# Kernel optimization log

Measured on AMD Instinct MI355X. Metric: run time of the kernel, lower is better.

The kernel has to match this reference:

```python
import jax, jax.numpy as jnp
import numpy as np

HID = 256  # hidden_dim in the torch module


def _graph_conv(h, edges, W0, b0, W1, b1):
    # pytorch3d.ops.GraphConv (undirected): out = w0(h) + sum_{neighbors} w1(h_nbr),
    # where each edge (i, j) contributes in both directions.
    out = h @ W0 + b0          # [V, H]
    nbr = h @ W1 + b1          # [V, H]
    i, j = edges[:, 0], edges[:, 1]
    out = out.at[i].add(nbr[j])
    out = out.at[j].add(nbr[i])
    return out


def setup_inputs() -> dict:
    key = jax.random.key(0)
    ks = jax.random.split(key, 16)
    V, E, F, H = 20496, 61440, 3840, HID  # 8 meshes x (2562 verts, 7680 edges); F = 256+512+1024+2048

    def w(k, shape):
        return jax.random.normal(k, shape, dtype=jnp.float32) * 0.02

    return {
        "vert_img_feats": jax.random.normal(ks[0], (V, F), dtype=jnp.float32),
        "verts": jax.random.normal(ks[1], (V, 3), dtype=jnp.float32),
        "edges": jax.random.randint(ks[2], (E, 2), 0, V),
        # bottleneck Linear(3840 -> 256)
        "Wb": w(ks[3], (F, H)), "bb": jnp.zeros((H,), jnp.float32),
        # GraphConv 0: input_dim = 3 + 256
        "W0_0": w(ks[4], (3 + H, H)), "b0_0": jnp.zeros((H,), jnp.float32),
        "W1_0": w(ks[5], (3 + H, H)), "b1_0": jnp.zeros((H,), jnp.float32),
        # GraphConv 1..9 stacked
        "gW0": w(ks[6], (9, H, H)), "gb0": jnp.zeros((9, H), jnp.float32),
        "gW1": w(ks[7], (9, H, H)), "gb1": jnp.zeros((9, H), jnp.float32),
        # vert_offset Linear(256 -> 3)
        "Wo": w(ks[8], (H, 3)), "bo": jnp.zeros((3,), jnp.float32),
        # asym_conf MLP: 256 -> 256 -> 64 -> 32 -> 1
        "A1": w(ks[9], (H, H)), "a1": jnp.zeros((H,), jnp.float32),
        "A2": w(ks[10], (H, 64)), "a2": jnp.zeros((64,), jnp.float32),
        "A3": w(ks[11], (64, 32)), "a3": jnp.zeros((32,), jnp.float32),
        "A4": w(ks[12], (32, 1)), "a4": jnp.zeros((1,), jnp.float32),
    }


def reference(vert_img_feats, verts, edges, Wb, bb, W0_0, b0_0, W1_0, b1_0,
              gW0, gb0, gW1, gb1, Wo, bo, A1, a1, A2, a2, A3, a3, A4, a4):
    # bottleneck + ReLU on per-vertex image features (vert_align output)
    h_img = jax.nn.relu(vert_img_feats @ Wb + bb)            # [V, 256]
    h = jnp.concatenate([h_img, verts], axis=1)              # [V, 259]
    h = jax.nn.relu(_graph_conv(h, edges, W0_0, b0_0, W1_0, b1_0))
    for k in range(9):  # fixed layer count, structurally distinct params
        h = jax.nn.relu(_graph_conv(h, edges, gW0[k], gb0[k], gW1[k], gb1[k]))
    delta_v = h @ Wo + bo                                    # [V, 3]
    z = jax.nn.relu(h @ A1 + a1)
    z = jax.nn.relu(z @ A2 + a2)
    z = jax.nn.relu(z @ A3 + a3)
    asym_conf = jax.nn.sigmoid(z @ A4 + a4)                  # [V, 1]
    return delta_v, asym_conf
```

## Files before the change

kernel.cpp:

```cpp
#include <hip/hip_runtime.h>

typedef _Float16 half8  __attribute__((ext_vector_type(8)));
typedef _Float16 half4v __attribute__((ext_vector_type(4)));
typedef float    floatx4 __attribute__((ext_vector_type(4)));

#define DEVINL __device__ __forceinline__

DEVINL void async_cp16(const void* g, void* l){
  __builtin_amdgcn_global_load_lds(
      (const __attribute__((address_space(1))) void*)g,
      (__attribute__((address_space(3))) void*)l,
      16, 0, 0);
}

DEVINL float wred64(float x){
  #pragma unroll
  for (int m = 32; m; m >>= 1) x += __shfl_xor(x, m, 64);
  return x;
}

__global__ __launch_bounds__(256) void k_gemm_bb(
    const float* __restrict__ A, const _Float16* __restrict__ BT,
    float* __restrict__ P, int M, int Mpad, int K, int lda, int kChunk)
{
  constexpr int BM = 128, BK = 32;
  __shared__ alignas(16) float    As[BM * BK];
  __shared__ alignas(16) _Float16 Bs[BM * BK];
  const int tid = threadIdx.x, wid = tid >> 6, lane = tid & 63;
  const int bm = blockIdx.x, bn = blockIdx.y, bz = blockIdx.z;
  const int kbeg = bz * kChunk, kend = kbeg + kChunk;

  const float* aSrc[4]; float* aDst[4];
  const int uSwA = (lane & 7) ^ ((lane >> 3) & 7);
  #pragma unroll
  for (int c = 0; c < 4; c++){
    int rloc = wid * 32 + c * 8 + (lane >> 3);
    int r = min(bm * BM + rloc, M - 1);
    aSrc[c] = A + (size_t)r * lda + uSwA * 4;
    aDst[c] = &As[(wid * 32 + c * 8) * BK];
  }
  const _Float16* bSrc[2]; _Float16* bDst[2];
  const int uSwB = (lane & 3) ^ ((lane >> 2) & 3);
  #pragma unroll
  for (int s = 0; s < 2; s++){
    int rb = bn * BM + (wid * 2 + s) * 16 + (lane >> 2);
    bSrc[s] = BT + (size_t)rb * K + uSwB * 8;
    bDst[s] = &Bs[(wid * 2 + s) * 16 * BK];
  }

  floatx4 acc[4][4];
  #pragma unroll
  for (int mt = 0; mt < 4; mt++)
    #pragma unroll
    for (int nt = 0; nt < 4; nt++) acc[mt][nt] = {0.f, 0.f, 0.f, 0.f};

  const int arow0 = (wid >> 1) * 64 + (lane & 15);
  const int g2 = (lane >> 4) * 2;
  const int a7 = lane & 7;
  const int brow0 = (wid & 1) * 64 + (lane & 15);
  const int ub = (lane >> 4) ^ (lane & 3);

  for (int k0 = kbeg; k0 < kend; k0 += BK){
    __syncthreads();
    #pragma unroll
    for (int c = 0; c < 4; c++) async_cp16(aSrc[c] + k0, aDst[c]);
    #pragma unroll
    for (int s = 0; s < 2; s++) async_cp16(bSrc[s] + k0, bDst[s]);
    __syncthreads();
    half8 af[4], bf[4];
    #pragma unroll
    for (int mt = 0; mt < 4; mt++){
      int arow = arow0 + mt * 16;
      floatx4 lo = *(const floatx4*)&As[arow * BK + ((g2    ) ^ a7) * 4];
      floatx4 hi = *(const floatx4*)&As[arow * BK + ((g2 + 1) ^ a7) * 4];
      #pragma unroll
      for (int j = 0; j < 4; j++){ af[mt][j] = (_Float16)lo[j]; af[mt][4+j] = (_Float16)hi[j]; }
    }
    #pragma unroll
    for (int nt = 0; nt < 4; nt++)
      bf[nt] = *(const half8*)&Bs[(brow0 + nt * 16) * BK + ub * 8];
    #pragma unroll
    for (int mt = 0; mt < 4; mt++)
      #pragma unroll
      for (int nt = 0; nt < 4; nt++)
        acc[mt][nt] = __builtin_amdgcn_mfma_f32_16x16x32_f16(af[mt], bf[nt], acc[mt][nt], 0, 0, 0);
  }

  const int colLocal = (wid & 1) * 64 + (lane & 15);
  const int rowLocal = (wid >> 1) * 64 + (lane >> 4) * 4;
  float* Pz = P + (size_t)bz * Mpad * 256;
  #pragma unroll
  for (int nt = 0; nt < 4; nt++){
    int col = bn * BM + colLocal + nt * 16;
    #pragma unroll
    for (int mt = 0; mt < 4; mt++){
      int r0 = bm * BM + rowLocal + mt * 16;
      #pragma unroll
      for (int i = 0; i < 4; i++)
        Pz[(size_t)(r0 + i) * 256 + col] = acc[mt][nt][i];
    }
  }
}

__global__ __launch_bounds__(256) void k_reduce(
    const float* __restrict__ P, const float* __restrict__ bias,
    _Float16* __restrict__ hA, int V, int Mpad)
{
  int idx = blockIdx.x * 256 + threadIdx.x;
  int base = idx * 4;
  int r = base >> 8, c = base & 255;
  const size_t stride = (size_t)Mpad * 256;
  const float* p = P + (size_t)r * 256 + c;
  floatx4 s0 = *(const floatx4*)(p);
  floatx4 s1 = *(const floatx4*)(p + stride);
  floatx4 s2 = *(const floatx4*)(p + 2 * stride);
  floatx4 s3 = *(const floatx4*)(p + 3 * stride);
  floatx4 b = *(const floatx4*)(bias + c);
  half4v o;
  if (r < V){
    #pragma unroll
    for (int e = 0; e < 4; e++)
      o[e] = (_Float16)fmaxf(s0[e] + s1[e] + s2[e] + s3[e] + b[e], 0.f);
  } else {
    #pragma unroll
    for (int e = 0; e < 4; e++) o[e] = (_Float16)0.f;
  }
  *(half4v*)(hA + (size_t)r * 256 + c) = o;
}

template<bool RELU, bool SPLIT, bool VERTC>
__global__ __launch_bounds__(256) void k_conv(
    const _Float16* __restrict__ A,
    const _Float16* __restrict__ BTfrag,
    const float* __restrict__ bias0, const float* __restrict__ bias1,
    const float* __restrict__ vertW, const float* __restrict__ verts,
    _Float16* __restrict__ C0, _Float16* __restrict__ C1, int Vreal)
{
  __shared__ alignas(16) _Float16 Bs[32768];
  const int tid = threadIdx.x, wid = tid >> 6, lane = tid & 63;
  const int bm = blockIdx.x, bn = blockIdx.y;

  const _Float16* src = BTfrag + (size_t)bn * 32768;
  #pragma unroll
  for (int jj = 0; jj < 16; jj++){
    int e = (jj * 256 + tid) * 8;
    *(half8*)&Bs[e] = *(const half8*)&src[e];
  }
  __syncthreads();

  const _Float16* Arow[4];
  #pragma unroll
  for (int mt = 0; mt < 4; mt++)
    Arow[mt] = A + (size_t)(bm * 128 + (wid >> 1) * 64 + mt * 16 + (lane & 15)) * 256
                 + (lane >> 4) * 8;
  const int nbase = (wid & 1) * 4;

  floatx4 acc[4][4];
  #pragma unroll
  for (int mt = 0; mt < 4; mt++)
    #pragma unroll
    for (int nt = 0; nt < 4; nt++) acc[mt][nt] = {0.f, 0.f, 0.f, 0.f};

  #pragma unroll
  for (int j = 0; j < 8; j++){
    half8 af[4], bf[4];
    #pragma unroll
    for (int mt = 0; mt < 4; mt++) af[mt] = *(const half8*)(Arow[mt] + j * 32);
    #pragma unroll
    for (int nt = 0; nt < 4; nt++)
      bf[nt] = *(const half8*)&Bs[(((nbase + nt) * 8 + j) * 64 + lane) * 8];
    #pragma unroll
    for (int mt = 0; mt < 4; mt++)
      #pragma unroll
      for (int nt = 0; nt < 4; nt++)
        acc[mt][nt] = __builtin_amdgcn_mfma_f32_16x16x32_f16(af[mt], bf[nt], acc[mt][nt], 0, 0, 0);
  }

  const int colLocal = (wid & 1) * 64 + (lane & 15);
  const int rowLocal = (wid >> 1) * 64 + (lane >> 4) * 4;
  #pragma unroll
  for (int nt = 0; nt < 4; nt++){
    int g = bn * 128 + colLocal + nt * 16;
    _Float16* Cp = C0;
    const float* bp = bias0;
    int col = g;
    if (SPLIT && g >= 256){ Cp = C1; bp = bias1; col = g - 256; }
    float b = bp[col];
    float w0 = 0.f, w1 = 0.f, w2 = 0.f;
    if (VERTC){ w0 = vertW[g*3+0]; w1 = vertW[g*3+1]; w2 = vertW[g*3+2]; }
    #pragma unroll
    for (int mt = 0; mt < 4; mt++){
      int r0 = bm * 128 + rowLocal + mt * 16;
      #pragma unroll
      for (int i = 0; i < 4; i++){
        int r = r0 + i;
        float v = acc[mt][nt][i] + b;
        if (VERTC){
          int vr = min(r, Vreal - 1);
          v += verts[vr*3+0] * w0 + verts[vr*3+1] * w1 + verts[vr*3+2] * w2;
        }
        if (RELU) v = fmaxf(v, 0.f);
        Cp[(size_t)r * 256 + col] = (_Float16)v;
      }
    }
  }
}

__global__ __launch_bounds__(256) void k_fill(const int* __restrict__ e, int E,
                                              int* __restrict__ cnt, int* __restrict__ adj){
  int t = blockIdx.x * 256 + threadIdx.x;
  if (t >= E) return;
  int i = e[t*2], j = e[t*2+1];
  int s = atomicAdd(&cnt[i], 1); if (s < 64) adj[(size_t)i*64 + s] = j;
  int q = atomicAdd(&cnt[j], 1); if (q < 64) adj[(size_t)j*64 + q] = i;
}

__global__ __launch_bounds__(256) void k_trans_bb(
    const float* __restrict__ Wb, _Float16* __restrict__ WbT)
{
  __shared__ float T[64][65];
  const int k0 = blockIdx.x * 64, n0 = blockIdx.y * 64;
  const int tr = threadIdx.x >> 6, tc = threadIdx.x & 63;
  #pragma unroll
  for (int i = 0; i < 16; i++){
    int rr = i * 4 + tr;
    T[rr][tc] = Wb[(size_t)(k0 + rr) * 256 + n0 + tc];
  }
  __syncthreads();
  #pragma unroll
  for (int i = 0; i < 16; i++){
    int rr = i * 4 + tr;
    WbT[(size_t)(n0 + rr) * 3840 + k0 + tc] = (_Float16)T[tc][rr];
  }
}

__global__ __launch_bounds__(256) void k_pack_frag(
    const float* __restrict__ W0_0, const float* __restrict__ W1_0,
    const float* __restrict__ gW0,  const float* __restrict__ gW1,
    const float* __restrict__ A1,
    _Float16* __restrict__ convB, _Float16* __restrict__ A1T,
    float* __restrict__ vertW)
{
  if (blockIdx.x == 672){
    for (int i = threadIdx.x; i < 1536; i += 256){
      int n = i / 3, c = i % 3;
      vertW[i] = (n < 256) ? W0_0[(size_t)(256 + c) * 256 + n]
                           : W1_0[(size_t)(256 + c) * 256 + (n - 256)];
    }
    return;
  }
  const int gw = blockIdx.x * 4 + (threadIdx.x >> 6);
  const int lane = threadIdx.x & 63;
  if (gw < 2560){
    int L = gw >> 8;
    int r = gw & 255;
    int n = (r >> 3) * 16 + (lane & 15);
    int k = (r & 7) * 32 + (lane >> 4) * 8;
    const float* W0 = L ? gW0 + (size_t)(L - 1) * 65536 : W0_0;
    const float* W1 = L ? gW1 + (size_t)(L - 1) * 65536 : W1_0;
    const float* Wsel = (n < 256) ? W0 : W1;
    int nn = n & 255;
    half8 v;
    #pragma unroll
    for (int e = 0; e < 8; e++) v[e] = (_Float16)Wsel[(size_t)(k + e) * 256 + nn];
    *(half8*)&convB[(size_t)L * 131072 + (size_t)r * 512 + lane * 8] = v;
  } else {
    int r = gw - 2560;
    int n = (r >> 3) * 16 + (lane & 15);
    int k = (r & 7) * 32 + (lane >> 4) * 8;
    half8 v;
    #pragma unroll
    for (int e = 0; e < 8; e++) v[e] = (_Float16)A1[(size_t)(k + e) * 256 + n];
    *(half8*)&A1T[(size_t)r * 512 + lane * 8] = v;
  }
}

__global__ __launch_bounds__(256) void k_gather(
    const _Float16* __restrict__ outB, const _Float16* __restrict__ nbrB,
    const int* __restrict__ cnt, const int* __restrict__ adj,
    _Float16* __restrict__ h, int V)
{
  int gw = (int)((blockIdx.x * 256 + threadIdx.x) >> 6);
  int lane = threadIdx.x & 63;
  if (gw >= V) return;
  half4v o = ((const half4v*)(outB + (size_t)gw * 256))[lane];
  float a0 = (float)o[0], a1 = (float)o[1], a2 = (float)o[2], a3 = (float)o[3];
  int n = min(cnt[gw], 64);
  const int* ap = adj + (size_t)gw * 64;
  int d = 0;
  for (; d + 1 < n; d += 2){
    int u0 = ap[d], u1 = ap[d+1];
    half4v x = ((const half4v*)(nbrB + (size_t)u0 * 256))[lane];
    half4v y = ((const half4v*)(nbrB + (size_t)u1 * 256))[lane];
    a0 += (float)x[0] + (float)y[0]; a1 += (float)x[1] + (float)y[1];
    a2 += (float)x[2] + (float)y[2]; a3 += (float)x[3] + (float)y[3];
  }
  if (d < n){
    int u = ap[d];
    half4v x = ((const half4v*)(nbrB + (size_t)u * 256))[lane];
    a0 += (float)x[0]; a1 += (float)x[1]; a2 += (float)x[2]; a3 += (float)x[3];
  }
  half4v rr;
  rr[0] = (_Float16)fmaxf(a0, 0.f); rr[1] = (_Float16)fmaxf(a1, 0.f);
  rr[2] = (_Float16)fmaxf(a2, 0.f); rr[3] = (_Float16)fmaxf(a3, 0.f);
  ((half4v*)(h + (size_t)gw * 256))[lane] = rr;
}

__global__ __launch_bounds__(1024) void k_head(
    const _Float16* __restrict__ hA, const _Float16* __restrict__ z1,
    const float* __restrict__ Wo, const float* __restrict__ bo,
    const float* __restrict__ A2, const float* __restrict__ a2,
    const float* __restrict__ A3, const float* __restrict__ a3,
    const float* __restrict__ A4, const float* __restrict__ a4,
    float* __restrict__ dOut, int V)
{
  __shared__ float A2s[256 * 64];
  __shared__ float A3s[64 * 32];
  __shared__ float Wos[768];
  __shared__ float zrow[16][256];
  __shared__ float z2s[16][64];
  const int tid = threadIdx.x;
  for (int i = tid; i < 256*64; i += 1024) A2s[i] = A2[i];
  for (int i = tid; i < 64*32;  i += 1024) A3s[i] = A3[i];
  if (tid < 768) Wos[tid] = Wo[tid];
  __syncthreads();
  const int wid = tid >> 6, lane = tid & 63;
  const int v = blockIdx.x * 16 + wid;
  if (v >= V) return;

  half4v hv = ((const half4v*)(hA + (size_t)v * 256))[lane];
  float hf[4] = { (float)hv[0], (float)hv[1], (float)hv[2], (float)hv[3] };
  float p0 = 0.f, p1 = 0.f, p2 = 0.f;
  int c0 = lane * 4;
  #pragma unroll
  for (int j = 0; j < 4; j++){
    p0 += hf[j] * Wos[(c0+j)*3 + 0];
    p1 += hf[j] * Wos[(c0+j)*3 + 1];
    p2 += hf[j] * Wos[(c0+j)*3 + 2];
  }
  p0 = wred64(p0); p1 = wred64(p1); p2 = wred64(p2);
  if (lane == 0){
    dOut[(size_t)v*3 + 0] = p0 + bo[0];
    dOut[(size_t)v*3 + 1] = p1 + bo[1];
    dOut[(size_t)v*3 + 2] = p2 + bo[2];
  }

  half4v zv = ((const half4v*)(z1 + (size_t)v * 256))[lane];
  floatx4 zf; zf[0] = (float)zv[0]; zf[1] = (float)zv[1]; zf[2] = (float)zv[2]; zf[3] = (float)zv[3];
  ((floatx4*)zrow[wid])[lane] = zf;
  __threadfence_block();
  float acc2 = a2[lane];
  #pragma unroll 4
  for (int c = 0; c < 256; c++) acc2 += zrow[wid][c] * A2s[c*64 + lane];
  acc2 = fmaxf(acc2, 0.f);
  z2s[wid][lane] = acc2;
  __threadfence_block();
  int o = lane & 31;
  float acc3 = a3[o];
  #pragma unroll 4
  for (int c = 0; c < 64; c++) acc3 += z2s[wid][c] * A3s[c*32 + o];
  acc3 = fmaxf(acc3, 0.f);
  float p = (lane < 32) ? acc3 * A4[lane] : 0.f;
  p = wred64(p);
  if (lane == 0){
    float s = 1.f / (1.f + expf(-(p + a4[0])));
    dOut[(size_t)V*3 + v] = s;
  }
}

extern "C" void kernel_launch(void* const* d_in, const int* in_sizes, int n_in,
                              void* d_out, int out_size, void* d_ws, size_t ws_size,
                              hipStream_t stream)
{
  const int V = 20496, E = 61440, F = 3840, Vpad = 20608;
  const float* X     = (const float*)d_in[0];
  const float* verts = (const float*)d_in[1];
  const int*   edges = (const int*)d_in[2];
  const float* Wb    = (const float*)d_in[3];
  const float* bbias = (const float*)d_in[4];
  const float* W0_0  = (const float*)d_in[5];
  const float* b0_0  = (const float*)d_in[6];
  const float* W1_0  = (const float*)d_in[7];
  const float* b1_0  = (const float*)d_in[8];
  const float* gW0   = (const float*)d_in[9];
  const float* gb0   = (const float*)d_in[10];
  const float* gW1   = (const float*)d_in[11];
  const float* gb1   = (const float*)d_in[12];
  const float* Wo    = (const float*)d_in[13];
  const float* bo    = (const float*)d_in[14];
  const float* A1    = (const float*)d_in[15];
  const float* a1    = (const float*)d_in[16];
  const float* A2    = (const float*)d_in[17];
  const float* a2    = (const float*)d_in[18];
  const float* A3    = (const float*)d_in[19];
  const float* a3    = (const float*)d_in[20];
  const float* A4    = (const float*)d_in[21];
  const float* a4    = (const float*)d_in[22];

  char* w = (char*)d_ws;
  const size_t SA = (size_t)Vpad * 256 * 2;
  _Float16* hA    = (_Float16*)(w);
  _Float16* outB  = (_Float16*)(w + SA);
  _Float16* nbrB  = (_Float16*)(w + 2*SA);
  _Float16* z1    = (_Float16*)(w + 3*SA);
  size_t off = 4 * SA;
  float*    P     = (float*)(w + off);    off += (size_t)4 * Vpad * 256 * 4;
  _Float16* WbT   = (_Float16*)(w + off); off += (size_t)256*3840*2;
  _Float16* convB = (_Float16*)(w + off); off += (size_t)10*131072*2;
  _Float16* A1T   = (_Float16*)(w + off); off += (size_t)131072*2;
  float*    vertW = (float*)(w + off);    off += (size_t)1536*4;
  int*      cnt   = (int*)(w + off);      off += (size_t)V*4;
  int*      adj   = (int*)(w + off);

  hipMemsetAsync(cnt, 0, (size_t)V*4, stream);

  k_fill<<<dim3((E + 255)/256), dim3(256), 0, stream>>>(edges, E, cnt, adj);
  k_trans_bb<<<dim3(60, 4), dim3(256), 0, stream>>>(Wb, WbT);
  k_pack_frag<<<dim3(673), dim3(256), 0, stream>>>(
      W0_0, W1_0, gW0, gW1, A1, convB, A1T, vertW);

  k_gemm_bb<<<dim3(161, 2, 4), dim3(256), 0, stream>>>(X, WbT, P, V, Vpad, F, F, 960);
  k_reduce<<<dim3(Vpad * 64 / 256), dim3(256), 0, stream>>>(P, bbias, hA, V, Vpad);

  for (int l = 0; l < 10; l++){
    const float* bp0 = l ? gb0 + (size_t)(l-1)*256 : b0_0;
    const float* bp1 = l ? gb1 + (size_t)(l-1)*256 : b1_0;
    const _Float16* Bt = convB + (size_t)l * 131072;
    if (l == 0)
      k_conv<false, true, true><<<dim3(161, 4), dim3(256), 0, stream>>>(
          hA, Bt, bp0, bp1, vertW, verts, outB, nbrB, V);
    else
      k_conv<false, true, false><<<dim3(161, 4), dim3(256), 0, stream>>>(
          hA, Bt, bp0, bp1, nullptr, nullptr, outB, nbrB, V);
    k_gather<<<dim3(5124), dim3(256), 0, stream>>>(outB, nbrB, cnt, adj, hA, V);
  }

  k_conv<true, false, false><<<dim3(161, 2), dim3(256), 0, stream>>>(
      hA, A1T, a1, nullptr, nullptr, nullptr, z1, nullptr, V);

  k_head<<<dim3(V/16), dim3(1024), 0, stream>>>(
      hA, z1, Wo, bo, A2, a2, A3, a3, A4, a4, (float*)d_out, V);
}
```

Measured before the change: 991.6 us.

## Widen bottleneck GEMM tile to full N, store fp16 partials, LDS-transpose weight packing

The bottleneck GEMM now computes all 256 output columns per block, so the large fp32 feature matrix is streamed and converted once instead of twice. Split-K partial sums are written in fp16, halving partial-buffer traffic in both the GEMM and the reduce kernel. Weight fragment packing is rewritten to stage weights through a shared-memory transpose with coalesced loads. The wider tile doubles accumulator registers per thread, which risks spills or lower occupancy, and fp16 partials reduce accumulation precision.

```diff
diff --git a/kernel.cpp b/kernel.cpp
--- a/kernel.cpp
+++ b/kernel.cpp
@@ -19,15 +19,15 @@
   return x;
 }
 
-__global__ __launch_bounds__(256) void k_gemm_bb(
+__global__ __launch_bounds__(256, 2) void k_gemm_bb(
     const float* __restrict__ A, const _Float16* __restrict__ BT,
-    float* __restrict__ P, int M, int Mpad, int K, int lda, int kChunk)
+    _Float16* __restrict__ P, int M, int Mpad, int K, int lda, int kChunk)
 {
   constexpr int BM = 128, BK = 32;
   __shared__ alignas(16) float    As[BM * BK];
-  __shared__ alignas(16) _Float16 Bs[BM * BK];
+  __shared__ alignas(16) _Float16 Bs[256 * BK];
   const int tid = threadIdx.x, wid = tid >> 6, lane = tid & 63;
-  const int bm = blockIdx.x, bn = blockIdx.y, bz = blockIdx.z;
+  const int bm = blockIdx.x, bz = blockIdx.z;
   const int kbeg = bz * kChunk, kend = kbeg + kChunk;
 
   const float* aSrc[4]; float* aDst[4];
@@ -37,37 +37,37 @@
     int rloc = wid * 32 + c * 8 + (lane >> 3);
     int r = min(bm * BM + rloc, M - 1);
     aSrc[c] = A + (size_t)r * lda + uSwA * 4;
-    aDst[c] = &As[(wid * 32 + c * 8) * BK];
-  }
-  const _Float16* bSrc[2]; _Float16* bDst[2];
+    aDst[c] = &As[rloc * BK];
+  }
+  const _Float16* bSrc[4]; _Float16* bDst[4];
   const int uSwB = (lane & 3) ^ ((lane >> 2) & 3);
   #pragma unroll
-  for (int s = 0; s < 2; s++){
-    int rb = bn * BM + (wid * 2 + s) * 16 + (lane >> 2);
-    bSrc[s] = BT + (size_t)rb * K + uSwB * 8;
-    bDst[s] = &Bs[(wid * 2 + s) * 16 * BK];
-  }
-
-  floatx4 acc[4][4];
+  for (int s = 0; s < 4; s++){
+    int rloc = wid * 64 + s * 16 + (lane >> 2);
+    bSrc[s] = BT + (size_t)rloc * K + uSwB * 8;
+    bDst[s] = &Bs[rloc * BK];
+  }
+
+  floatx4 acc[4][8];
   #pragma unroll
   for (int mt = 0; mt < 4; mt++)
     #pragma unroll
-    for (int nt = 0; nt < 4; nt++) acc[mt][nt] = {0.f, 0.f, 0.f, 0.f};
+    for (int nt = 0; nt < 8; nt++) acc[mt][nt] = {0.f, 0.f, 0.f, 0.f};
 
   const int arow0 = (wid >> 1) * 64 + (lane & 15);
   const int g2 = (lane >> 4) * 2;
   const int a7 = lane & 7;
-  const int brow0 = (wid & 1) * 64 + (lane & 15);
-  const int ub = (lane >> 4) ^ (lane & 3);
+  const int brow0 = (wid & 1) * 128 + (lane & 15);
+  const int ub0 = lane >> 4;
 
   for (int k0 = kbeg; k0 < kend; k0 += BK){
     __syncthreads();
     #pragma unroll
     for (int c = 0; c < 4; c++) async_cp16(aSrc[c] + k0, aDst[c]);
     #pragma unroll
-    for (int s = 0; s < 2; s++) async_cp16(bSrc[s] + k0, bDst[s]);
+    for (int s = 0; s < 4; s++) async_cp16(bSrc[s] + k0, bDst[s]);
     __syncthreads();
-    half8 af[4], bf[4];
+    half8 af[4], bf[8];
     #pragma unroll
     for (int mt = 0; mt < 4; mt++){
       int arow = arow0 + mt * 16;
@@ -77,55 +77,58 @@
       for (int j = 0; j < 4; j++){ af[mt][j] = (_Float16)lo[j]; af[mt][4+j] = (_Float16)hi[j]; }
     }
     #pragma unroll
-    for (int nt = 0; nt < 4; nt++)
-      bf[nt] = *(const half8*)&Bs[(brow0 + nt * 16) * BK + ub * 8];
+    for (int nt = 0; nt < 8; nt++){
+      int brow = brow0 + nt * 16;
+      bf[nt] = *(const half8*)&Bs[brow * BK + (ub0 ^ (brow & 3)) * 8];
+    }
     #pragma unroll
     for (int mt = 0; mt < 4; mt++)
       #pragma unroll
-      for (int nt = 0; nt < 4; nt++)
+      for (int nt = 0; nt < 8; nt++)
         acc[mt][nt] = __builtin_amdgcn_mfma_f32_16x16x32_f16(af[mt], bf[nt], acc[mt][nt], 0, 0, 0);
   }
 
-  const int colLocal = (wid & 1) * 64 + (lane & 15);
+  const int colLocal = (wid & 1) * 128 + (lane & 15);
   const int rowLocal = (wid >> 1) * 64 + (lane >> 4) * 4;
-  float* Pz = P + (size_t)bz * Mpad * 256;
-  #pragma unroll
-  for (int nt = 0; nt < 4; nt++){
-    int col = bn * BM + colLocal + nt * 16;
+  _Float16* Pz = P + (size_t)bz * Mpad * 256;
+  #pragma unroll
+  for (int nt = 0; nt < 8; nt++){
+    int col = colLocal + nt * 16;
     #pragma unroll
     for (int mt = 0; mt < 4; mt++){
       int r0 = bm * BM + rowLocal + mt * 16;
       #pragma unroll
       for (int i = 0; i < 4; i++)
-        Pz[(size_t)(r0 + i) * 256 + col] = acc[mt][nt][i];
+        Pz[(size_t)(r0 + i) * 256 + col] = (_Float16)acc[mt][nt][i];
     }
   }
 }
 
 __global__ __launch_bounds__(256) void k_reduce(
-    const float* __restrict__ P, const float* __restrict__ bias,
+    const _Float16* __restrict__ P, const float* __restrict__ bias,
     _Float16* __restrict__ hA, int V, int Mpad)
 {
   int idx = blockIdx.x * 256 + threadIdx.x;
-  int base = idx * 4;
+  int base = idx * 8;
   int r = base >> 8, c = base & 255;
   const size_t stride = (size_t)Mpad * 256;
-  const float* p = P + (size_t)r * 256 + c;
-  floatx4 s0 = *(const floatx4*)(p);
-  floatx4 s1 = *(const floatx4*)(p + stride);
-  floatx4 s2 = *(const floatx4*)(p + 2 * stride);
-  floatx4 s3 = *(const floatx4*)(p + 3 * stride);
-  floatx4 b = *(const floatx4*)(bias + c);
-  half4v o;
+  const _Float16* p = P + (size_t)base;
+  half8 s0 = *(const half8*)(p);
+  half8 s1 = *(const half8*)(p + stride);
+  half8 s2 = *(const half8*)(p + 2 * stride);
+  half8 s3 = *(const half8*)(p + 3 * stride);
+  half8 o;
   if (r < V){
     #pragma unroll
-    for (int e = 0; e < 4; e++)
-      o[e] = (_Float16)fmaxf(s0[e] + s1[e] + s2[e] + s3[e] + b[e], 0.f);
+    for (int e = 0; e < 8; e++){
+      float v = (float)s0[e] + (float)s1[e] + (float)s2[e] + (float)s3[e] + bias[c + e];
+      o[e] = (_Float16)fmaxf(v, 0.f);
+    }
   } else {
     #pragma unroll
-    for (int e = 0; e < 4; e++) o[e] = (_Float16)0.f;
-  }
-  *(half4v*)(hA + (size_t)r * 256 + c) = o;
+    for (int e = 0; e < 8; e++) o[e] = (_Float16)0.f;
+  }
+  *(half8*)(hA + (size_t)base) = o;
 }
 
 template<bool RELU, bool SPLIT, bool VERTC>
@@ -234,14 +237,16 @@
   }
 }
 
-__global__ __launch_bounds__(256) void k_pack_frag(
+__global__ __launch_bounds__(256) void k_pack2(
     const float* __restrict__ W0_0, const float* __restrict__ W1_0,
     const float* __restrict__ gW0,  const float* __restrict__ gW1,
     const float* __restrict__ A1,
     _Float16* __restrict__ convB, _Float16* __restrict__ A1T,
     float* __restrict__ vertW)
 {
-  if (blockIdx.x == 672){
+  __shared__ float T[64 * 257];
+  const int b = blockIdx.x;
+  if (b == 84){
     for (int i = threadIdx.x; i < 1536; i += 256){
       int n = i / 3, c = i % 3;
       vertW[i] = (n < 256) ? W0_0[(size_t)(256 + c) * 256 + n]
@@ -249,29 +254,38 @@
     }
     return;
   }
-  const int gw = blockIdx.x * 4 + (threadIdx.x >> 6);
-  const int lane = threadIdx.x & 63;
-  if (gw < 2560){
-    int L = gw >> 8;
-    int r = gw & 255;
-    int n = (r >> 3) * 16 + (lane & 15);
-    int k = (r & 7) * 32 + (lane >> 4) * 8;
-    const float* W0 = L ? gW0 + (size_t)(L - 1) * 65536 : W0_0;
-    const float* W1 = L ? gW1 + (size_t)(L - 1) * 65536 : W1_0;
-    const float* Wsel = (n < 256) ? W0 : W1;
-    int nn = n & 255;
+  const int m = b >> 2, t = b & 3;
+  const float* W; _Float16* dstBase; int rAdd;
+  if (m == 20){ W = A1; dstBase = A1T; rAdd = 0; }
+  else {
+    int L = m >> 1, hsel = m & 1;
+    W = hsel ? (L ? gW1 + (size_t)(L-1)*65536 : W1_0)
+             : (L ? gW0 + (size_t)(L-1)*65536 : W0_0);
+    dstBase = convB + (size_t)L * 131072;
+    rAdd = hsel * 128;
+  }
+  const int k0 = t * 64;
+  const int tr = threadIdx.x >> 6, tc = (threadIdx.x & 63) * 4;
+  #pragma unroll
+  for (int i = 0; i < 16; i++){
+    int rr = i * 4 + tr;
+    floatx4 v = *(const floatx4*)&W[(size_t)(k0 + rr) * 256 + tc];
+    T[rr * 257 + tc + 0] = v[0]; T[rr * 257 + tc + 1] = v[1];
+    T[rr * 257 + tc + 2] = v[2]; T[rr * 257 + tc + 3] = v[3];
+  }
+  __syncthreads();
+  const int wid = threadIdx.x >> 6, lane = threadIdx.x & 63;
+  #pragma unroll
+  for (int q = 0; q < 8; q++){
+    int n16 = wid * 4 + (q >> 1);
+    int jj  = q & 1;
+    int r = rAdd + n16 * 8 + (t * 2 + jj);
+    int kk = jj * 32 + (lane >> 4) * 8;
+    int n  = n16 * 16 + (lane & 15);
     half8 v;
     #pragma unroll
-    for (int e = 0; e < 8; e++) v[e] = (_Float16)Wsel[(size_t)(k + e) * 256 + nn];
-    *(half8*)&convB[(size_t)L * 131072 + (size_t)r * 512 + lane * 8] = v;
-  } else {
-    int r = gw - 2560;
-    int n = (r >> 3) * 16 + (lane & 15);
-    int k = (r & 7) * 32 + (lane >> 4) * 8;
-    half8 v;
-    #pragma unroll
-    for (int e = 0; e < 8; e++) v[e] = (_Float16)A1[(size_t)(k + e) * 256 + n];
-    *(half8*)&A1T[(size_t)r * 512 + lane * 8] = v;
+    for (int e = 0; e < 8; e++) v[e] = (_Float16)T[(kk + e) * 257 + n];
+    *(half8*)&dstBase[(size_t)r * 512 + lane * 8] = v;
   }
 }
 
@@ -404,7 +418,7 @@
   _Float16* nbrB  = (_Float16*)(w + 2*SA);
   _Float16* z1    = (_Float16*)(w + 3*SA);
   size_t off = 4 * SA;
-  float*    P     = (float*)(w + off);    off += (size_t)4 * Vpad * 256 * 4;
+  _Float16* P     = (_Float16*)(w + off); off += (size_t)4 * Vpad * 256 * 2;
   _Float16* WbT   = (_Float16*)(w + off); off += (size_t)256*3840*2;
   _Float16* convB = (_Float16*)(w + off); off += (size_t)10*131072*2;
   _Float16* A1T   = (_Float16*)(w + off); off += (size_t)131072*2;
@@ -416,11 +430,11 @@
 
   k_fill<<<dim3((E + 255)/256), dim3(256), 0, stream>>>(edges, E, cnt, adj);
   k_trans_bb<<<dim3(60, 4), dim3(256), 0, stream>>>(Wb, WbT);
-  k_pack_frag<<<dim3(673), dim3(256), 0, stream>>>(
+  k_pack2<<<dim3(85), dim3(256), 0, stream>>>(
       W0_0, W1_0, gW0, gW1, A1, convB, A1T, vertW);
 
-  k_gemm_bb<<<dim3(161, 2, 4), dim3(256), 0, stream>>>(X, WbT, P, V, Vpad, F, F, 960);
-  k_reduce<<<dim3(Vpad * 64 / 256), dim3(256), 0, stream>>>(P, bbias, hA, V, Vpad);
+  k_gemm_bb<<<dim3(161, 1, 4), dim3(256), 0, stream>>>(X, WbT, P, V, Vpad, F, F, 960);
+  k_reduce<<<dim3(Vpad / 8), dim3(256), 0, stream>>>(P, bbias, hA, V, Vpad);
 
   for (int l = 0; l < 10; l++){
     const float* bp0 = l ? gb0 + (size_t)(l-1)*256 : b0_0;
```

Result: no change. 979.3 us (-1.2%).
